# Kernel optimization log

Hardware: AMD Instinct MI355X
Metric: run time of the kernel (lower is better)

The kernel has to match this reference:

```python
import jax, jax.numpy as jnp
import numpy as np

N_EXPERTS = 8  # matches init n_experts


def _dispatch(x, expert_weights, top_experts, bias):
    """Faithful port of Experts.forward: sort tokens by expert, binned_gather
    into [E, capacity, d] with capacity-based token dropping, binned_scatter
    back weighted by expert_weights, then add bias. (The shown source never
    applies self.expert inside permute_and_compute, so the expert compute is
    identity; cond/mask are gathered then discarded and do not affect output.)"""
    b, n, d = x.shape
    top_k = top_experts.shape[-1]
    T = b * n * top_k
    # expert_capacity = int(top_k * tokens / n_experts)  (static)
    C = (top_k * b * n) // N_EXPERTS
    te = top_experts.reshape(-1).astype(jnp.int32)          # [T]
    w = expert_weights.reshape(-1)                           # [T]
    # ops.sort (stable radix sort over expert ids)
    order = jnp.argsort(te, stable=True)                     # indices [T]
    bin_ids = te[order]                                      # sorted expert ids
    # ops.histogram + inclusive_cumsum -> bin starts
    tpe = jnp.zeros((N_EXPERTS,), jnp.int32).at[te].add(1)   # tokens_per_expert
    starts = jnp.cumsum(tpe) - tpe                           # exclusive cumsum
    pos = jnp.arange(T, dtype=jnp.int32) - starts[bin_ids]   # position in bin
    valid = pos < C                                          # capacity drop
    slot = bin_ids * C + pos                                 # flat [E*C] slot
    tok = order // top_k                                     # source token row
    xf = x.reshape(-1, d)
    # binned_gather: [E*C, d], invalid entries routed to a dummy row
    gathered = (jnp.zeros((N_EXPERTS * C + 1, d), x.dtype)
                .at[jnp.where(valid, slot, N_EXPERTS * C)].set(xf[tok]))[:N_EXPERTS * C]
    # binned_scatter: out[tok] += w * gathered[slot] for valid entries
    wv = jnp.where(valid, w[order], jnp.zeros((), w.dtype))
    out = (jnp.zeros((b * n, d), x.dtype)
           .at[tok].add(wv[:, None] * gathered[jnp.where(valid, slot, 0)]))
    return out.reshape(b, n, d) + bias


def setup_inputs() -> dict:
    key = jax.random.key(0)
    k = jax.random.split(key, 6)
    b, n, d, dc, top_k = 4, 4096, 1024, 256, 2
    x = jax.random.normal(k[0], (b, n, d), jnp.float32)
    cond = jax.random.normal(k[1], (b, n, dc), jnp.float32)
    mask = jnp.ones((b, n), jnp.bool_)
    scores = jax.random.uniform(k[2], (b, n, N_EXPERTS), jnp.float32)
    expert_weights = jax.random.uniform(k[3], (b, n, top_k), jnp.float32)
    top_experts = jax.random.randint(k[4], (b, n, top_k), 0, N_EXPERTS, jnp.int32)
    bias = jax.random.normal(k[5], (d,), jnp.float32)
    return {"x": x, "cond": cond, "mask": mask, "scores": scores,
            "expert_weights": expert_weights, "top_experts": top_experts,
            "bias": bias}


def reference(x, cond, mask, scores, expert_weights, top_experts, bias):
    return _dispatch(x, expert_weights, top_experts, bias)
```

## Files before the change

kernel.cpp:

```cpp
#include <hip/hip_runtime.h>

#define N_EXPERTS 8
#define ROWS_PB 8
#define ENT_PB 16
#define MAGIC 0x9E3779B9u
typedef unsigned long long u64;
typedef unsigned int u32;
typedef float f32x4 __attribute__((ext_vector_type(4)));
typedef int i32x4 __attribute__((ext_vector_type(4)));

__device__ __forceinline__ void packed_add(u64& c0, u64& c1, int e) {
  if (e < 4) c0 += 1ull << (16 * e);
  else       c1 += 1ull << (16 * (e - 4));
}
__device__ __forceinline__ void packed_add_val(u64& c0, u64& c1, int e, int v) {
  if (e < 4) c0 += (u64)v << (16 * e);
  else       c1 += (u64)v << (16 * (e - 4));
}
__device__ __forceinline__ int packed_get(u64 c0, u64 c1, int e) {
  return (e < 4) ? (int)((c0 >> (16 * e)) & 0xFFFF)
                 : (int)((c1 >> (16 * (e - 4))) & 0xFFFF);
}

__global__ __launch_bounds__(256) void fused_kernel(
    const float* __restrict__ x, const int* __restrict__ te,
    const float* __restrict__ ew, const float* __restrict__ bias,
    float* __restrict__ out, u64* __restrict__ h64, int C, int nsb) {
  __shared__ u64 w0s[4], w1s[4];
  __shared__ int ids_s[ENT_PB];
  __shared__ float scale_s[ROWS_PB];
  const int tid = threadIdx.x;
  const int lane = tid & 63, wid = tid >> 6;
  const int b = blockIdx.x;
  const int E0 = b * ENT_PB;
  const int sb = b >> 6;
  const int partial4 = 4 * (b & 63);

  const i32x4* __restrict__ te4 = reinterpret_cast<const i32x4*>(te);

  if (b < nsb) {
    const i32x4 v = te4[b * 256 + tid];
    u64 a0 = 0, a1 = 0;
    packed_add(a0, a1, v.x & 7);
    packed_add(a0, a1, v.y & 7);
    packed_add(a0, a1, v.z & 7);
    packed_add(a0, a1, v.w & 7);
#pragma unroll
    for (int m = 1; m < 64; m <<= 1) {
      a0 += __shfl_xor(a0, m);
      a1 += __shfl_xor(a1, m);
    }
    if (lane == 0) { w0s[wid] = a0; w1s[wid] = a1; }
    __syncthreads();
    if (tid < N_EXPERTS) {
      int cnt = 0;
#pragma unroll
      for (int ww = 0; ww < 4; ++ww) cnt += packed_get(w0s[ww], w1s[ww], tid);
      const u64 pk = ((u64)(((u32)cnt) ^ MAGIC) << 32) | (u32)cnt;
      __hip_atomic_store(&h64[b * N_EXPERTS + tid], pk, __ATOMIC_RELEASE,
                         __HIP_MEMORY_SCOPE_AGENT);
    }
    __syncthreads();
  }

  const f32x4* __restrict__ x4 =
      reinterpret_cast<const f32x4*>(x) + b * (ROWS_PB * 256);
  f32x4 xv0 = x4[0 * 256 + tid], xv1 = x4[1 * 256 + tid];
  f32x4 xv2 = x4[2 * 256 + tid], xv3 = x4[3 * 256 + tid];
  f32x4 xv4 = x4[4 * 256 + tid], xv5 = x4[5 * 256 + tid];
  f32x4 xv6 = x4[6 * 256 + tid], xv7 = x4[7 * 256 + tid];
  const f32x4 bv = reinterpret_cast<const f32x4*>(bias)[tid];

  int myid = 0;
  float myw = 0.f;
  if (tid < ENT_PB) {
    myid = te[E0 + tid] & 7;
    myw = ew[E0 + tid];
  }

  u64 c0 = 0, c1 = 0;
  {
    const int bb = tid >> 3;
    if (bb < sb) {
      u64 pk;
      int guard = 0;
      do {
        pk = __hip_atomic_load(&h64[tid], __ATOMIC_RELAXED,
                               __HIP_MEMORY_SCOPE_AGENT);
        if ((u32)(pk >> 32) == (((u32)pk) ^ MAGIC)) break;
        __builtin_amdgcn_s_sleep(2);
      } while (++guard < (1 << 22));
      packed_add_val(c0, c1, tid & 7, (int)(u32)pk);
    }
  }
  if (tid < partial4) {
    const i32x4 v = te4[sb * 256 + tid];
    packed_add(c0, c1, v.x & 7);
    packed_add(c0, c1, v.y & 7);
    packed_add(c0, c1, v.z & 7);
    packed_add(c0, c1, v.w & 7);
  }
#pragma unroll
  for (int m = 1; m < 64; m <<= 1) {
    c0 += __shfl_xor(c0, m);
    c1 += __shfl_xor(c1, m);
  }
  if (lane == 0) { w0s[wid] = c0; w1s[wid] = c1; }
  if (tid < ENT_PB) ids_s[tid] = myid;
  __syncthreads();

  if (tid < ENT_PB) {
    const u64 p0 = w0s[0] + w0s[1] + w0s[2] + w0s[3];
    const u64 p1 = w1s[0] + w1s[1] + w1s[2] + w1s[3];
    int r = packed_get(p0, p1, myid);
#pragma unroll
    for (int j = 0; j < ENT_PB - 1; ++j)
      r += (j < tid) & (ids_s[j] == myid);
    float contrib = (r < C) ? myw : 0.f;
    const float pair = contrib + __shfl_xor(contrib, 1);
    if ((tid & 1) == 0) scale_s[tid >> 1] = pair;
  }
  __syncthreads();

  f32x4* __restrict__ o4 = reinterpret_cast<f32x4*>(out) + b * (ROWS_PB * 256);
  {
    float s;
    f32x4 ov;
#define EMIT(K, XV)                                   \
    s = scale_s[K];                                   \
    ov = XV * s + bv;                                 \
    __builtin_nontemporal_store(ov, &o4[K * 256 + tid]);
    EMIT(0, xv0) EMIT(1, xv1) EMIT(2, xv2) EMIT(3, xv3)
    EMIT(4, xv4) EMIT(5, xv5) EMIT(6, xv6) EMIT(7, xv7)
#undef EMIT
  }
}

extern "C" void kernel_launch(void* const* d_in, const int* in_sizes, int n_in,
                              void* d_out, int out_size, void* d_ws,
                              size_t ws_size, hipStream_t stream) {
  const float* x    = (const float*)d_in[0];
  const float* ew   = (const float*)d_in[4];
  const int*   te   = (const int*)d_in[5];
  const float* bias = (const float*)d_in[6];
  float* out = (float*)d_out;
  u64* h64 = (u64*)d_ws;

  const int T = in_sizes[5];
  const int C = T / N_EXPERTS;
  const int nsb = T / 1024;
  const int nblocks = (in_sizes[0] / 1024) / ROWS_PB;

  fused_kernel<<<nblocks, 256, 0, stream>>>(x, te, ew, bias, out, h64, C, nsb);
}
```

Measured before the change: 25.71 us.

## Add a second stage computing per-token scales in dedicated blocks

```diff
diff --git a/kernel.cpp b/kernel.cpp
--- a/kernel.cpp
+++ b/kernel.cpp
@@ -2,7 +2,7 @@
 
 #define N_EXPERTS 8
 #define ROWS_PB 8
-#define ENT_PB 16
+#define NSB 32
 #define MAGIC 0x9E3779B9u
 typedef unsigned long long u64;
 typedef unsigned int u32;
@@ -13,32 +13,46 @@
   if (e < 4) c0 += 1ull << (16 * e);
   else       c1 += 1ull << (16 * (e - 4));
 }
-__device__ __forceinline__ void packed_add_val(u64& c0, u64& c1, int e, int v) {
-  if (e < 4) c0 += (u64)v << (16 * e);
-  else       c1 += (u64)v << (16 * (e - 4));
-}
 __device__ __forceinline__ int packed_get(u64 c0, u64 c1, int e) {
   return (e < 4) ? (int)((c0 >> (16 * e)) & 0xFFFF)
                  : (int)((c1 >> (16 * (e - 4))) & 0xFFFF);
 }
 
+__device__ __forceinline__ u64 pack_ck(u32 v) {
+  return ((u64)(v ^ MAGIC) << 32) | v;
+}
+__device__ __forceinline__ bool ck_ok(u64 pk) {
+  return (u32)(pk >> 32) == (((u32)pk) ^ MAGIC);
+}
+__device__ __forceinline__ u32 spin_load(const u64* p) {
+  u64 pk = *p;
+  if (!ck_ok(pk)) {
+    int guard = 0;
+    do {
+      pk = __hip_atomic_load(p, __ATOMIC_RELAXED, __HIP_MEMORY_SCOPE_AGENT);
+      if (ck_ok(pk)) break;
+      __builtin_amdgcn_s_sleep(2);
+    } while (++guard < (1 << 22));
+  }
+  return (u32)pk;
+}
+
 __global__ __launch_bounds__(256) void fused_kernel(
     const float* __restrict__ x, const int* __restrict__ te,
     const float* __restrict__ ew, const float* __restrict__ bias,
-    float* __restrict__ out, u64* __restrict__ h64, int C, int nsb) {
+    float* __restrict__ out, u64* __restrict__ h64, u64* __restrict__ s64,
+    int C) {
+  __shared__ int histl[NSB * N_EXPERTS];
+  __shared__ int bpre[N_EXPERTS];
   __shared__ u64 w0s[4], w1s[4];
-  __shared__ int ids_s[ENT_PB];
   __shared__ float scale_s[ROWS_PB];
   const int tid = threadIdx.x;
   const int lane = tid & 63, wid = tid >> 6;
   const int b = blockIdx.x;
-  const int E0 = b * ENT_PB;
-  const int sb = b >> 6;
-  const int partial4 = 4 * (b & 63);
+  const i32x4* __restrict__ te4 = reinterpret_cast<const i32x4*>(te);
+  const f32x4* __restrict__ ew4 = reinterpret_cast<const f32x4*>(ew);
 
-  const i32x4* __restrict__ te4 = reinterpret_cast<const i32x4*>(te);
-
-  if (b < nsb) {
+  if (b < NSB) {
     const i32x4 v = te4[b * 256 + tid];
     u64 a0 = 0, a1 = 0;
     packed_add(a0, a1, v.x & 7);
@@ -56,11 +70,52 @@
       int cnt = 0;
 #pragma unroll
       for (int ww = 0; ww < 4; ++ww) cnt += packed_get(w0s[ww], w1s[ww], tid);
-      const u64 pk = ((u64)(((u32)cnt) ^ MAGIC) << 32) | (u32)cnt;
-      __hip_atomic_store(&h64[b * N_EXPERTS + tid], pk, __ATOMIC_RELEASE,
-                         __HIP_MEMORY_SCOPE_AGENT);
+      __hip_atomic_store(&h64[b * N_EXPERTS + tid], pack_ck((u32)cnt),
+                         __ATOMIC_RELEASE, __HIP_MEMORY_SCOPE_AGENT);
     }
     __syncthreads();
+  } else if (b < 2 * NSB) {
+    const int sbb = b - NSB;
+    const i32x4 v = te4[sbb * 256 + tid];
+    const f32x4 w = ew4[sbb * 256 + tid];
+
+    histl[tid] = (int)spin_load(&h64[tid]);
+    __syncthreads();
+    if (tid < N_EXPERTS) {
+      int s = 0;
+      for (int bb = 0; bb < sbb; ++bb) s += histl[bb * N_EXPERTS + tid];
+      bpre[tid] = s;
+    }
+
+    const int e0 = v.x & 7, e1 = v.y & 7, e2 = v.z & 7, e3 = v.w & 7;
+    u64 c0 = 0, c1 = 0;
+    packed_add(c0, c1, e0);
+    packed_add(c0, c1, e1);
+    packed_add(c0, c1, e2);
+    packed_add(c0, c1, e3);
+    u64 s0 = c0, s1 = c1;
+#pragma unroll
+    for (int i = 1; i < 64; i <<= 1) {
+      u64 t0 = __shfl_up(s0, i), t1 = __shfl_up(s1, i);
+      if (lane >= i) { s0 += t0; s1 += t1; }
+    }
+    u64 x0 = s0 - c0, x1 = s1 - c1;
+    if (lane == 63) { w0s[wid] = s0; w1s[wid] = s1; }
+    __syncthreads();
+    for (int ww = 0; ww < wid; ++ww) { x0 += w0s[ww]; x1 += w1s[ww]; }
+
+    const int r0 = bpre[e0] + packed_get(x0, x1, e0);
+    const int r1 = bpre[e1] + packed_get(x0, x1, e1) + (e1 == e0);
+    const int r2 = bpre[e2] + packed_get(x0, x1, e2) + (e2 == e0) + (e2 == e1);
+    const int r3 = bpre[e3] + packed_get(x0, x1, e3) + (e3 == e0) +
+                   (e3 == e1) + (e3 == e2);
+    const float sa = (r0 < C ? w.x : 0.f) + (r1 < C ? w.y : 0.f);
+    const float sb = (r2 < C ? w.z : 0.f) + (r3 < C ? w.w : 0.f);
+    const int tok2 = (sbb * 256 + tid) * 2;
+    __hip_atomic_store(&s64[tok2], pack_ck(__float_as_uint(sa)),
+                       __ATOMIC_RELEASE, __HIP_MEMORY_SCOPE_AGENT);
+    __hip_atomic_store(&s64[tok2 + 1], pack_ck(__float_as_uint(sb)),
+                       __ATOMIC_RELEASE, __HIP_MEMORY_SCOPE_AGENT);
   }
 
   const f32x4* __restrict__ x4 =
@@ -71,55 +126,8 @@
   f32x4 xv6 = x4[6 * 256 + tid], xv7 = x4[7 * 256 + tid];
   const f32x4 bv = reinterpret_cast<const f32x4*>(bias)[tid];
 
-  int myid = 0;
-  float myw = 0.f;
-  if (tid < ENT_PB) {
-    myid = te[E0 + tid] & 7;
-    myw = ew[E0 + tid];
-  }
-
-  u64 c0 = 0, c1 = 0;
-  {
-    const int bb = tid >> 3;
-    if (bb < sb) {
-      u64 pk;
-      int guard = 0;
-      do {
-        pk = __hip_atomic_load(&h64[tid], __ATOMIC_RELAXED,
-                               __HIP_MEMORY_SCOPE_AGENT);
-        if ((u32)(pk >> 32) == (((u32)pk) ^ MAGIC)) break;
-        __builtin_amdgcn_s_sleep(2);
-      } while (++guard < (1 << 22));
-      packed_add_val(c0, c1, tid & 7, (int)(u32)pk);
-    }
-  }
-  if (tid < partial4) {
-    const i32x4 v = te4[sb * 256 + tid];
-    packed_add(c0, c1, v.x & 7);
-    packed_add(c0, c1, v.y & 7);
-    packed_add(c0, c1, v.z & 7);
-    packed_add(c0, c1, v.w & 7);
-  }
-#pragma unroll
-  for (int m = 1; m < 64; m <<= 1) {
-    c0 += __shfl_xor(c0, m);
-    c1 += __shfl_xor(c1, m);
-  }
-  if (lane == 0) { w0s[wid] = c0; w1s[wid] = c1; }
-  if (tid < ENT_PB) ids_s[tid] = myid;
-  __syncthreads();
-
-  if (tid < ENT_PB) {
-    const u64 p0 = w0s[0] + w0s[1] + w0s[2] + w0s[3];
-    const u64 p1 = w1s[0] + w1s[1] + w1s[2] + w1s[3];
-    int r = packed_get(p0, p1, myid);
-#pragma unroll
-    for (int j = 0; j < ENT_PB - 1; ++j)
-      r += (j < tid) & (ids_s[j] == myid);
-    float contrib = (r < C) ? myw : 0.f;
-    const float pair = contrib + __shfl_xor(contrib, 1);
-    if ((tid & 1) == 0) scale_s[tid >> 1] = pair;
-  }
+  if (tid < ROWS_PB)
+    scale_s[tid] = __uint_as_float(spin_load(&s64[b * ROWS_PB + tid]));
   __syncthreads();
 
   f32x4* __restrict__ o4 = reinterpret_cast<f32x4*>(out) + b * (ROWS_PB * 256);
@@ -145,11 +153,11 @@
   const float* bias = (const float*)d_in[6];
   float* out = (float*)d_out;
   u64* h64 = (u64*)d_ws;
+  u64* s64 = (u64*)d_ws + NSB * N_EXPERTS;
 
   const int T = in_sizes[5];
   const int C = T / N_EXPERTS;
-  const int nsb = T / 1024;
   const int nblocks = (in_sizes[0] / 1024) / ROWS_PB;
 
-  fused_kernel<<<nblocks, 256, 0, stream>>>(x, te, ew, bias, out, h64, C, nsb);
+  fused_kernel<<<nblocks, 256, 0, stream>>>(x, te, ew, bias, out, h64, s64, C);
 }
```

Result: slower. 33.31 us (+29.6%).
